# Kernel optimization log

Hardware: AMD Instinct MI355X
Metric: run time of the kernel (lower is better)

The kernel has to match this reference:

```python
import jax, jax.numpy as jnp
import numpy as np

SHIFT_MIN, SHIFT_MAX = -14.0, 0.0  # weight_bits=5 -> (-(2^4-2), 0)
FRAC_BITS = 16
INT_BITS = 16


def round_to_fixed(x):
    # deepshift utils.round_to_fixed: floor to 2^-16 grid, clamp to [-2^15, 2^15-1]
    delta = 2.0 ** (-FRAC_BITS)
    bound = 2.0 ** (INT_BITS - 1)
    r = jnp.floor(x / delta) * delta
    return jnp.clip(r, -bound, bound - 1)


def setup_inputs() -> dict:
    key = jax.random.key(0)
    k1, k2, k3, k4 = jax.random.split(key, 4)
    N, IN, OUT = 524288, 128, 128
    x = jax.random.normal(k1, (N, IN), dtype=jnp.float32)
    shift = jax.random.uniform(k2, (OUT, IN), dtype=jnp.float32, minval=SHIFT_MIN, maxval=SHIFT_MAX)
    sign = jax.random.uniform(k3, (OUT, IN), dtype=jnp.float32, minval=-1.0, maxval=1.0)
    bound = 1.0 / np.sqrt(IN)
    bias = jax.random.uniform(k4, (OUT,), dtype=jnp.float32, minval=-bound, maxval=bound)
    return {"input": x, "shift": shift, "sign": sign, "bias": bias}


def reference(input, shift, sign, bias):
    # quantize weights: v = 2^round(clamp(shift)) * sign(round(sign))
    shift_r = jnp.round(jnp.clip(shift, SHIFT_MIN, SHIFT_MAX))
    sign_s = jnp.sign(jnp.round(sign))
    v = jnp.exp2(shift_r) * sign_s  # [OUT, IN]
    x_q = round_to_fixed(input)
    b_q = round_to_fixed(bias)
    # F.linear: x @ v.T + b
    return jnp.dot(x_q, v.T) + b_q[None, :]
```

## Files before the change

### kernel.cpp

```cpp
#include <hip/hip_runtime.h>
#include <hip/hip_bf16.h>
#include <stdint.h>

typedef __attribute__((ext_vector_type(4)))  float f32x4;
typedef __attribute__((ext_vector_type(16))) float f32x16;
typedef __attribute__((ext_vector_type(8)))  short bf16x8;

constexpr int IN_DIM  = 128;
constexpr int OUT_DIM = 128;
constexpr int BLOCK   = 256;
constexpr int TILE_ROWS = 32;
constexpr int TILES_PER_BLOCK = 8;
constexpr int ROWS_PER_BLOCK = TILE_ROWS * TILES_PER_BLOCK;
constexpr int NBUF = 2;

__device__ __forceinline__ bf16x8 build_seg(const float* __restrict__ shiftp,
                                            const float* __restrict__ signp,
                                            int row, int j)
{
    const int g = row * IN_DIM + j * 8;
    f32x4 sh0 = *reinterpret_cast<const f32x4*>(shiftp + g);
    f32x4 sh1 = *reinterpret_cast<const f32x4*>(shiftp + g + 4);
    f32x4 sg0 = *reinterpret_cast<const f32x4*>(signp + g);
    f32x4 sg1 = *reinterpret_cast<const f32x4*>(signp + g + 4);
    union { ushort u[8]; bf16x8 v; } tmp;
    #pragma unroll
    for (int e = 0; e < 8; ++e) {
        float sh = (e < 4) ? sh0[e] : sh1[e - 4];
        float sg = (e < 4) ? sg0[e] : sg1[e - 4];
        sh = fminf(fmaxf(sh, -14.0f), 0.0f);
        const int   si = (int)rintf(sh);
        const float rs = rintf(sg);
        ushort bits = 0;
        if (rs != 0.0f)
            bits = (ushort)(((rs < 0.0f) ? 0x8000u : 0u) |
                            (unsigned)((127 + si) << 7));
        tmp.u[e] = bits;
    }
    return tmp.v;
}

__device__ __forceinline__ void stage_tile(const float* __restrict__ gtile,
                                           float* __restrict__ lbuf,
                                           int wave, int lane)
{
    #pragma unroll
    for (int i = 0; i < 4; ++i) {
        const int seg = wave * 4 + i;
        const int p   = seg * 64 + lane;
        const int row = p >> 5;
        const int cl  = p & 31;
        const int cg  = cl ^ (row & 7);
        const float* g = gtile + row * IN_DIM + cg * 4;
        __builtin_amdgcn_global_load_lds(
            (const __attribute__((address_space(1))) unsigned int*)(uintptr_t)g,
            (__attribute__((address_space(3))) unsigned int*)(uintptr_t)(lbuf + seg * 256),
            16, 0, 0);
    }
}

__global__ __launch_bounds__(BLOCK, 3)
void linshift_main(const float* __restrict__ x,
                   const float* __restrict__ shiftp,
                   const float* __restrict__ signp,
                   const float* __restrict__ biasp,
                   float* __restrict__ out)
{
    __shared__ float xbuf[NBUF][TILE_ROWS * IN_DIM];

    const int t    = threadIdx.x;
    const int ct   = t >> 6;
    const int lane = t & 63;
    const int ml   = lane & 31;
    const int hi   = lane >> 5;
    const int o    = ct * 32 + ml;

    bf16x8 vb[8];
    #pragma unroll
    for (int ks = 0; ks < 8; ++ks)
        vb[ks] = build_seg(shiftp, signp, o, ks * 2 + hi);
    const float bv = floorf(biasp[o] * 65536.0f) * (1.0f / 65536.0f);

    const long long brow0 = (long long)blockIdx.x * ROWS_PER_BLOCK;
    const float* xblock = x + brow0 * IN_DIM;

    stage_tile(xblock, xbuf[0], ct, lane);

    const int swz = ml & 7;
    #pragma unroll
    for (int tl = 0; tl < TILES_PER_BLOCK; ++tl) {
        if (tl == 0) asm volatile("s_waitcnt vmcnt(0)"  ::: "memory");
        else         asm volatile("s_waitcnt vmcnt(16)" ::: "memory");
        __builtin_amdgcn_s_barrier();
        __builtin_amdgcn_sched_barrier(0);

        if (tl + 1 < TILES_PER_BLOCK)
            stage_tile(xblock + (long long)(tl + 1) * TILE_ROWS * IN_DIM,
                       xbuf[(tl + 1) & 1], ct, lane);

        const float* buf = xbuf[tl & 1];

        bf16x8 a[8];
        #pragma unroll
        for (int ks = 0; ks < 8; ++ks) {
            const int c0 = ks * 4 + hi * 2;
            f32x4 f0 = *reinterpret_cast<const f32x4*>(&buf[ml * IN_DIM + ((c0 ^ swz) << 2)]);
            f32x4 f1 = *reinterpret_cast<const f32x4*>(&buf[ml * IN_DIM + (((c0 + 1) ^ swz) << 2)]);
            union { ushort u[8]; bf16x8 v; } tmp;
            #pragma unroll
            for (int e = 0; e < 4; ++e) {
                __hip_bfloat16 h0 = __float2bfloat16(f0[e]);
                __hip_bfloat16 h1 = __float2bfloat16(f1[e]);
                tmp.u[e]     = *reinterpret_cast<const ushort*>(&h0);
                tmp.u[e + 4] = *reinterpret_cast<const ushort*>(&h1);
            }
            a[ks] = tmp.v;
        }

        f32x16 acc;
        #pragma unroll
        for (int r = 0; r < 16; ++r) acc[r] = bv;
        #pragma unroll
        for (int ks = 0; ks < 8; ++ks)
            acc = __builtin_amdgcn_mfma_f32_32x32x16_bf16(a[ks], vb[ks], acc, 0, 0, 0);

        float* op = out + (brow0 + (long long)tl * TILE_ROWS) * OUT_DIM + o;
        #pragma unroll
        for (int r = 0; r < 16; ++r) {
            const int m = (r & 3) + 8 * (r >> 2) + 4 * hi;
            __builtin_nontemporal_store(acc[r], op + m * OUT_DIM);
        }
        __builtin_amdgcn_sched_barrier(0);
    }
}

extern "C" void kernel_launch(void* const* d_in, const int* in_sizes, int n_in,
                              void* d_out, int out_size, void* d_ws, size_t ws_size,
                              hipStream_t stream) {
    const float* x  = (const float*)d_in[0];
    const float* sh = (const float*)d_in[1];
    const float* sg = (const float*)d_in[2];
    const float* b  = (const float*)d_in[3];
    float* out = (float*)d_out;

    const int N = in_sizes[0] / IN_DIM;
    const int grid = N / ROWS_PER_BLOCK;
    linshift_main<<<grid, BLOCK, 0, stream>>>(x, sh, sg, b, out);
}
```

Measured before the change: 97.47 us.

## Load input rows directly from global memory instead of LDS double-buffering

Drops the global_load_lds staging of x tiles into a swizzled, double-buffered shared-memory ring, along with the explicit vmcnt waits and barriers. Each wave now reads its 32 input rows straight from global memory with 16-byte vector loads, using the same k-column mapping as before. This removes the barrier synchronisation and the LDS traffic. The cost is that all four waves in a block fetch the same x rows, so the block issues four times as many x requests, which must be absorbed by L1/L2. Cross-tile prefetching is also lost, and latency hiding now depends on the compiler and on occupancy.

Measured after the change: 169.0 us. +73.3%, slower.

```diff
diff --git a/kernel.cpp b/kernel.cpp
--- a/kernel.cpp
+++ b/kernel.cpp
@@ -9,10 +9,9 @@
 constexpr int IN_DIM  = 128;
 constexpr int OUT_DIM = 128;
 constexpr int BLOCK   = 256;
-constexpr int TILE_ROWS = 32;
-constexpr int TILES_PER_BLOCK = 8;
-constexpr int ROWS_PER_BLOCK = TILE_ROWS * TILES_PER_BLOCK;
-constexpr int NBUF = 2;
+constexpr int CHUNK_ROWS = 32;
+constexpr int CHUNKS_PER_BLOCK = 8;
+constexpr int ROWS_PER_BLOCK = CHUNK_ROWS * CHUNKS_PER_BLOCK;
 
 __device__ __forceinline__ bf16x8 build_seg(const float* __restrict__ shiftp,
                                             const float* __restrict__ signp,
@@ -40,25 +39,6 @@
     return tmp.v;
 }
 
-__device__ __forceinline__ void stage_tile(const float* __restrict__ gtile,
-                                           float* __restrict__ lbuf,
-                                           int wave, int lane)
-{
-    #pragma unroll
-    for (int i = 0; i < 4; ++i) {
-        const int seg = wave * 4 + i;
-        const int p   = seg * 64 + lane;
-        const int row = p >> 5;
-        const int cl  = p & 31;
-        const int cg  = cl ^ (row & 7);
-        const float* g = gtile + row * IN_DIM + cg * 4;
-        __builtin_amdgcn_global_load_lds(
-            (const __attribute__((address_space(1))) unsigned int*)(uintptr_t)g,
-            (__attribute__((address_space(3))) unsigned int*)(uintptr_t)(lbuf + seg * 256),
-            16, 0, 0);
-    }
-}
-
 __global__ __launch_bounds__(BLOCK, 3)
 void linshift_main(const float* __restrict__ x,
                    const float* __restrict__ shiftp,
@@ -66,8 +46,6 @@
                    const float* __restrict__ biasp,
                    float* __restrict__ out)
 {
-    __shared__ float xbuf[NBUF][TILE_ROWS * IN_DIM];
-
     const int t    = threadIdx.x;
     const int ct   = t >> 6;
     const int lane = t & 63;
@@ -82,30 +60,16 @@
     const float bv = floorf(biasp[o] * 65536.0f) * (1.0f / 65536.0f);
 
     const long long brow0 = (long long)blockIdx.x * ROWS_PER_BLOCK;
-    const float* xblock = x + brow0 * IN_DIM;
 
-    stage_tile(xblock, xbuf[0], ct, lane);
-
-    const int swz = ml & 7;
-    #pragma unroll
-    for (int tl = 0; tl < TILES_PER_BLOCK; ++tl) {
-        if (tl == 0) asm volatile("s_waitcnt vmcnt(0)"  ::: "memory");
-        else         asm volatile("s_waitcnt vmcnt(16)" ::: "memory");
-        __builtin_amdgcn_s_barrier();
-        __builtin_amdgcn_sched_barrier(0);
-
-        if (tl + 1 < TILES_PER_BLOCK)
-            stage_tile(xblock + (long long)(tl + 1) * TILE_ROWS * IN_DIM,
-                       xbuf[(tl + 1) & 1], ct, lane);
-
-        const float* buf = xbuf[tl & 1];
+    for (int c = 0; c < CHUNKS_PER_BLOCK; ++c) {
+        const long long r0 = brow0 + (long long)c * CHUNK_ROWS;
+        const float* xp = x + (r0 + ml) * IN_DIM + hi * 8;
 
         bf16x8 a[8];
         #pragma unroll
         for (int ks = 0; ks < 8; ++ks) {
-            const int c0 = ks * 4 + hi * 2;
-            f32x4 f0 = *reinterpret_cast<const f32x4*>(&buf[ml * IN_DIM + ((c0 ^ swz) << 2)]);
-            f32x4 f1 = *reinterpret_cast<const f32x4*>(&buf[ml * IN_DIM + (((c0 + 1) ^ swz) << 2)]);
+            f32x4 f0 = *reinterpret_cast<const f32x4*>(xp + ks * 16);
+            f32x4 f1 = *reinterpret_cast<const f32x4*>(xp + ks * 16 + 4);
             union { ushort u[8]; bf16x8 v; } tmp;
             #pragma unroll
             for (int e = 0; e < 4; ++e) {
@@ -124,13 +88,12 @@
         for (int ks = 0; ks < 8; ++ks)
             acc = __builtin_amdgcn_mfma_f32_32x32x16_bf16(a[ks], vb[ks], acc, 0, 0, 0);
 
-        float* op = out + (brow0 + (long long)tl * TILE_ROWS) * OUT_DIM + o;
+        float* op = out + r0 * OUT_DIM + o;
         #pragma unroll
         for (int r = 0; r < 16; ++r) {
             const int m = (r & 3) + 8 * (r >> 2) + 4 * hi;
             __builtin_nontemporal_store(acc[r], op + m * OUT_DIM);
         }
-        __builtin_amdgcn_sched_barrier(0);
     }
 }
 
```
